# Performance work log

Hardware: AMD Instinct MI355X
Metric: run time of the kernel (lower is better)

## Reference

```python
import jax, jax.numpy as jnp
import numpy as np

B, D, T, R = 8, 128, 32768, 2
C = D // R  # reduced channel dim = 64


def conv1x1(x, w, b):
    # x: [B, Cin, T], w: [Cout, Cin], b: [Cout] -> [B, Cout, T]
    return jnp.einsum('oi,bit->bot', w, x) + b[None, :, None]


def setup_inputs() -> dict:
    key = jax.random.key(0)
    ks = jax.random.split(key, 16)
    inp = {
        'x1': jax.random.normal(ks[0], (B, D, T), dtype=jnp.float32),
        'x2': jnp.zeros((B, D, T), dtype=jnp.float32),  # unused in encoder stage
        'mask': jnp.ones((B, 1, T), dtype=jnp.float32),
        # 1x1 conv projections (weights squeezed to [out, in])
        'wq': jax.random.normal(ks[1], (C, D), dtype=jnp.float32) * 0.05,
        'bq': jnp.zeros((C,), dtype=jnp.float32),
        'wk': jax.random.normal(ks[2], (C, D), dtype=jnp.float32) * 0.05,
        'bk': jnp.zeros((C,), dtype=jnp.float32),
        'wv': jax.random.normal(ks[3], (C, D), dtype=jnp.float32) * 0.05,
        'bv': jnp.zeros((C,), dtype=jnp.float32),
        # E, F: Linear(C -> C) with bias
        'we': jax.random.normal(ks[4], (C, C), dtype=jnp.float32) * 0.1,
        'be': jnp.zeros((C,), dtype=jnp.float32),
        'wf': jax.random.normal(ks[5], (C, C), dtype=jnp.float32) * 0.1,
        'bf': jnp.zeros((C,), dtype=jnp.float32),
        # output 1x1 conv: C -> D
        'wo': jax.random.normal(ks[6], (D, C), dtype=jnp.float32) * 0.05,
        'bo': jnp.zeros((D,), dtype=jnp.float32),
    }
    return inp


def reference(x1, x2, mask, wq, bq, wk, bk, wv, bv, we, be, wf, bf, wo, bo):
    # Q/K/V projections (encoder stage: value from x1; x2 unused)
    Q = conv1x1(x1, wq, bq)              # [B, C, T]
    K = conv1x1(x1, wk, bk)              # [B, C, T]
    V = conv1x1(x1, wv, bv)              # [B, C, T]
    # K = E(K^T): [B, T, C] @ we^T + be
    Kp = jnp.einsum('bct,oc->bto', K, we) + be  # [B, T, C]
    # S = Q @ Kp -> [B, C, C], scaled by sqrt(last dim)
    S = jnp.einsum('bct,btk->bck', Q, Kp)
    P = jax.nn.softmax(S / jnp.sqrt(jnp.asarray(S.shape[-1], S.dtype)), axis=-1)
    # dropout is identity in eval mode
    # V = (F(V^T))^T: [B, C, T]
    Vp = jnp.einsum('bct,oc->bot', V, wf) + bf[None, :, None]  # [B, C, T]
    out = jnp.einsum('bck,bkt->bct', P, Vp)  # [B, C, T]
    out = conv1x1(jax.nn.relu(out), wo, bo)  # [B, D, T]
    return out * mask[:, 0:1, :]
```

## Files before the change

kernel.cpp:

```cpp
#include <hip/hip_runtime.h>
#include <stdint.h>
#include <stddef.h>

#define B_ 8
#define D_ 128
#define T_ 32768
#define C_ 64
#define NCH_ 128

typedef __bf16 bf16;
typedef __bf16 bf16x4 __attribute__((ext_vector_type(4)));
typedef __bf16 bf16x8 __attribute__((ext_vector_type(8)));
typedef float f32x2 __attribute__((ext_vector_type(2)));
typedef float f32x4 __attribute__((ext_vector_type(4)));
typedef float f32x16 __attribute__((ext_vector_type(16)));

__device__ __forceinline__ f32x16 zero16() {
  f32x16 z;
#pragma unroll
  for (int i = 0; i < 16; ++i) z[i] = 0.f;
  return z;
}

__global__ __launch_bounds__(256) void k0_zero(float* __restrict__ p, int n)
{
  int i = blockIdx.x * 256 + threadIdx.x;
  if (i < n) p[i] = 0.f;
}

__global__ __launch_bounds__(256, 2) void k1_gram(
    const float* __restrict__ x1,
    const float* __restrict__ we, const float* __restrict__ wk,
    const float* __restrict__ bk, const float* __restrict__ be,
    const float* __restrict__ wf, const float* __restrict__ wv,
    const float* __restrict__ bv, const float* __restrict__ bfv,
    const float* __restrict__ wo,
    float* __restrict__ G, float* __restrict__ r,
    float* __restrict__ wkp, float* __restrict__ wvp,
    float* __restrict__ bkp, float* __restrict__ bvp,
    bf16* __restrict__ wobf,
    float* __restrict__ gpart)
{
  const int blk = blockIdx.x;
  const int tid = threadIdx.x;
  const int ngram = B_ * NCH_;

  if (blk >= ngram) {
    const int wb = blk - ngram;
    if (wb < 64) {
      const float* wa  = (wb < 32) ? we : wf;
      const float* wb2 = (wb < 32) ? wk : wv;
      float* outw      = (wb < 32) ? wkp : wvp;
      const int idx = (wb & 31) * 256 + tid;
      const int o = idx >> 7, d = idx & 127;
      float s = 0.f;
      for (int c = 0; c < 64; ++c) s += wa[o * 64 + c] * wb2[c * 128 + d];
      outw[idx] = s;
      if (tid < 64) {
        if (wb == 0) {
          float t = 0.f;
          for (int c = 0; c < 64; ++c) t += we[tid * 64 + c] * bk[c];
          bkp[tid] = t + be[tid];
        } else if (wb == 32) {
          float t = 0.f;
          for (int c = 0; c < 64; ++c) t += wf[tid * 64 + c] * bv[c];
          bvp[tid] = t + bfv[tid];
        }
      }
    } else {
      const int idx = (wb - 64) * 256 + tid;
      wobf[idx] = (bf16)wo[idx];
    }
    return;
  }

  __shared__ bf16 x_s[128 * 264];

  const int b  = blk >> 7;
  const int ch = blk & (NCH_ - 1);
  const int t0 = ch * (T_ / NCH_);
  const int wave = tid >> 6, lane = tid & 63;
  const int lrow = lane & 31, lk = lane >> 5;
  const int qa = wave >> 1, qb = wave & 1;

  const float* xb = x1 + (size_t)b * D_ * T_ + t0;

#pragma unroll
  for (int g = 0; g < 4; ++g) {
    f32x4 pre[8];
#pragma unroll
    for (int i = 0; i < 8; ++i) {
      const int row = 32 * wave + 8 * g + i;
      pre[i] = *(const f32x4*)(xb + (size_t)row * T_ + 4 * lane);
    }
#pragma unroll
    for (int i = 0; i < 8; ++i) {
      const int row = 32 * wave + 8 * g + i;
      bf16x4 h;
#pragma unroll
      for (int j = 0; j < 4; ++j) h[j] = (bf16)pre[i][j];
      *(bf16x4*)&x_s[row * 264 + 4 * lane] = h;
    }
  }
  __syncthreads();

  f32x16 acc00 = zero16(), acc01 = zero16(), acc10 = zero16(), acc11 = zero16();
  float rsum = 0.f;

  const bf16* A0  = &x_s[(64 * qa + lrow) * 264 + 8 * lk];
  const bf16* A1  = A0 + 32 * 264;
  const bf16* Bb0 = &x_s[(64 * qb + lrow) * 264 + 8 * lk];
  const bf16* Bb1 = Bb0 + 32 * 264;

#pragma unroll
  for (int k = 0; k < 16; ++k) {
    bf16x8 fa0 = *(const bf16x8*)(A0 + 16 * k);
    bf16x8 fa1 = *(const bf16x8*)(A1 + 16 * k);
    bf16x8 fb0 = *(const bf16x8*)(Bb0 + 16 * k);
    bf16x8 fb1 = *(const bf16x8*)(Bb1 + 16 * k);
    bf16x8 own = qb ? fa1 : fa0;
#pragma unroll
    for (int j = 0; j < 8; ++j) rsum += (float)own[j];
    acc00 = __builtin_amdgcn_mfma_f32_32x32x16_bf16(fa0, fb0, acc00, 0, 0, 0);
    acc01 = __builtin_amdgcn_mfma_f32_32x32x16_bf16(fa0, fb1, acc01, 0, 0, 0);
    acc10 = __builtin_amdgcn_mfma_f32_32x32x16_bf16(fa1, fb0, acc10, 0, 0, 0);
    acc11 = __builtin_amdgcn_mfma_f32_32x32x16_bf16(fa1, fb1, acc11, 0, 0, 0);
  }

  if (gpart) {
    float* gp = gpart + (size_t)blk * 16384 + wave * 4096;
#pragma unroll
    for (int rr = 0; rr < 16; ++rr) {
      f32x4 v;
      v[0] = acc00[rr]; v[1] = acc01[rr]; v[2] = acc10[rr]; v[3] = acc11[rr];
      *(f32x4*)(gp + rr * 256 + lane * 4) = v;
    }
  } else {
    float* gb = G + (size_t)b * 16384;
#pragma unroll
    for (int rr = 0; rr < 16; ++rr) {
      const int rloc = (rr & 3) + 8 * (rr >> 2) + 4 * lk;
      const int r0 = 64 * qa + rloc, r1 = 64 * qa + 32 + rloc;
      const int c0 = 64 * qb + lrow, c1 = 64 * qb + 32 + lrow;
      atomicAdd(&gb[r0 * 128 + c0], acc00[rr]);
      atomicAdd(&gb[r0 * 128 + c1], acc01[rr]);
      atomicAdd(&gb[r1 * 128 + c0], acc10[rr]);
      atomicAdd(&gb[r1 * 128 + c1], acc11[rr]);
    }
  }
  float rtot = rsum + __shfl_xor(rsum, 32, 64);
  if (lk == 0) atomicAdd(&r[b * 128 + 32 * wave + lrow], rtot);
}

__global__ __launch_bounds__(256) void k2_reduce(
    const float* __restrict__ gpart, float* __restrict__ G)
{
  const int g4 = blockIdx.x * 256 + threadIdx.x;
  const int b = g4 >> 12;
  const int e4 = g4 & 4095;
  const f32x4* p = (const f32x4*)(gpart + ((size_t)b * NCH_) * 16384) + e4;
  f32x4 s = {0.f, 0.f, 0.f, 0.f};
#pragma unroll 8
  for (int ch = 0; ch < NCH_; ++ch) s += p[(size_t)ch * 4096];

  const int w = e4 >> 10, rr = (e4 >> 6) & 15, lane = e4 & 63;
  const int lk = lane >> 5, lrow = lane & 31;
  const int qa = w >> 1, qb = w & 1;
  const int rloc = (rr & 3) + 8 * (rr >> 2) + 4 * lk;
  const int r0 = 64 * qa + rloc, c0 = 64 * qb + lrow;
  float* Gb = G + (size_t)b * 16384;
  Gb[r0 * 128 + c0]               = s[0];
  Gb[r0 * 128 + c0 + 32]          = s[1];
  Gb[(r0 + 32) * 128 + c0]        = s[2];
  Gb[(r0 + 32) * 128 + c0 + 32]   = s[3];
}

__global__ __launch_bounds__(128) void k3_softmax(
    const float* __restrict__ wq, const float* __restrict__ bq,
    const float* __restrict__ G, const float* __restrict__ r,
    const float* __restrict__ wkp, const float* __restrict__ wvp,
    const float* __restrict__ bkp, const float* __restrict__ bvp,
    bf16* __restrict__ attw, float* __restrict__ attb)
{
  const int b = blockIdx.x >> 6, c = blockIdx.x & 63;
  const int tid = threadIdx.x;
  __shared__ float sM[128], sR[128], sQ[128], sP[64];
  __shared__ float sRed;

  const float* Gb = G + (size_t)b * 16384;
  const float* wqc = wq + c * 128;

  const float rv = r[b * 128 + tid];
  sR[tid] = rv;
  float m = 0.f;
  for (int j = 0; j < 128; ++j) m += wqc[j] * Gb[j * 128 + tid];
  sM[tid] = m;
  sQ[tid] = wqc[tid] * rv;
  __syncthreads();

  if (tid < 64) {
    float q2 = sQ[tid] + sQ[tid + 64];
#pragma unroll
    for (int off = 32; off; off >>= 1) q2 += __shfl_xor(q2, off, 64);
    if (tid == 0) sRed = q2;
  }
  __syncthreads();
  const float qr = sRed;
  const float bqc = bq[c];

  if (tid < 64) {
    const int k = tid;
    float s = 0.f, wkr = 0.f;
    for (int i = 0; i < 128; ++i) {
      const float w = wkp[k * 128 + i];
      s += sM[i] * w;
      wkr += sR[i] * w;
    }
    const float bk2 = bkp[k];
    float logit = (s + bqc * wkr + bk2 * qr + (float)T_ * bqc * bk2) * 0.125f;
    float mx = logit;
#pragma unroll
    for (int off = 32; off; off >>= 1) mx = fmaxf(mx, __shfl_xor(mx, off, 64));
    const float e = __expf(logit - mx);
    float sum = e;
#pragma unroll
    for (int off = 32; off; off >>= 1) sum += __shfl_xor(sum, off, 64);
    sP[k] = e / sum;
  }
  __syncthreads();

  {
    float aw = 0.f;
    for (int k = 0; k < 64; ++k) aw += sP[k] * wvp[k * 128 + tid];
    attw[((size_t)b * 64 + c) * 128 + tid] = (bf16)aw;
  }
  if (tid < 64) {
    float pb = sP[tid] * bvp[tid];
#pragma unroll
    for (int off = 32; off; off >>= 1) pb += __shfl_xor(pb, off, 64);
    if (tid == 0) attb[b * 64 + c] = pb;
  }
}

__global__ __launch_bounds__(256, 2) void k4_out(
    const float* __restrict__ x1, const float* __restrict__ mask,
    const bf16* __restrict__ wobf, const float* __restrict__ bo,
    const bf16* __restrict__ attw, const float* __restrict__ attb,
    float* __restrict__ out)
{
  __shared__ __attribute__((aligned(16))) char buf[128 * 136 * 2];
  bf16*  x_st = (bf16*)buf;
  float* o_s  = (float*)buf;
  __shared__ bf16 m1t[128 * 72];
  __shared__ float bo_s[128];
  __shared__ float ab_s[64];

  const int b = blockIdx.x >> 8;
  const int t0 = (blockIdx.x & 255) << 7;
  const int tid = threadIdx.x;
  const int wave = tid >> 6, lane = tid & 63;
  const int lrow = lane & 31, lk = lane >> 5;

  if (tid < 128) bo_s[tid] = bo[tid];
  if (tid < 64) ab_s[tid] = attb[b * 64 + tid];

  const float* xb = x1 + (size_t)b * D_ * T_ + t0;
#pragma unroll
  for (int g = 0; g < 4; ++g) {
    f32x2 pr[8];
#pragma unroll
    for (int i = 0; i < 8; ++i) {
      const int d = 32 * wave + 8 * g + i;
      pr[i] = *(const f32x2*)(xb + (size_t)d * T_ + 2 * lane);
    }
#pragma unroll
    for (int i = 0; i < 8; ++i) {
      const int d = 32 * wave + 8 * g + i;
      x_st[(2 * lane) * 136 + d]     = (bf16)pr[i][0];
      x_st[(2 * lane + 1) * 136 + d] = (bf16)pr[i][1];
    }
  }
  __syncthreads();

  const bf16* awb = attw + (size_t)b * 8192;
  f32x16 m0 = zero16(), m1a = zero16();
  const bf16* ax = &x_st[(32 * wave + lrow) * 136 + 8 * lk];
#pragma unroll
  for (int ki = 0; ki < 8; ++ki) {
    bf16x8 af = *(const bf16x8*)(ax + 16 * ki);
    bf16x8 b0 = *(const bf16x8*)(awb + (size_t)lrow * 128 + 16 * ki + 8 * lk);
    bf16x8 b1 = *(const bf16x8*)(awb + (size_t)(32 + lrow) * 128 + 16 * ki + 8 * lk);
    m0  = __builtin_amdgcn_mfma_f32_32x32x16_bf16(af, b0, m0, 0, 0, 0);
    m1a = __builtin_amdgcn_mfma_f32_32x32x16_bf16(af, b1, m1a, 0, 0, 0);
  }
#pragma unroll
  for (int rr = 0; rr < 16; ++rr) {
    const int tl = 32 * wave + (rr & 3) + 8 * (rr >> 2) + 4 * lk;
    m1t[tl * 72 + lrow]      = (bf16)fmaxf(m0[rr]  + ab_s[lrow], 0.f);
    m1t[tl * 72 + 32 + lrow] = (bf16)fmaxf(m1a[rr] + ab_s[32 + lrow], 0.f);
  }
  __syncthreads();

  f32x16 q0 = zero16(), q1 = zero16(), q2 = zero16(), q3 = zero16();
  const bf16* mrow = &m1t[(32 * wave + lrow) * 72];
#pragma unroll
  for (int k0 = 0; k0 < 4; ++k0) {
    bf16x8 bm = *(const bf16x8*)(mrow + 16 * k0 + 8 * lk);
    bf16x8 w0 = *(const bf16x8*)(wobf + (size_t)(lrow) * 64 + 16 * k0 + 8 * lk);
    bf16x8 w1 = *(const bf16x8*)(wobf + (size_t)(32 + lrow) * 64 + 16 * k0 + 8 * lk);
    bf16x8 w2 = *(const bf16x8*)(wobf + (size_t)(64 + lrow) * 64 + 16 * k0 + 8 * lk);
    bf16x8 w3 = *(const bf16x8*)(wobf + (size_t)(96 + lrow) * 64 + 16 * k0 + 8 * lk);
    q0 = __builtin_amdgcn_mfma_f32_32x32x16_bf16(w0, bm, q0, 0, 0, 0);
    q1 = __builtin_amdgcn_mfma_f32_32x32x16_bf16(w1, bm, q1, 0, 0, 0);
    q2 = __builtin_amdgcn_mfma_f32_32x32x16_bf16(w2, bm, q2, 0, 0, 0);
    q3 = __builtin_amdgcn_mfma_f32_32x32x16_bf16(w3, bm, q3, 0, 0, 0);
  }

  const int tl = 32 * wave + lrow;
  const float mv = mask[(size_t)b * T_ + t0 + tl];
  float* ob = out + (size_t)b * D_ * T_ + t0;

#pragma unroll
  for (int rr = 0; rr < 16; ++rr) {
    const int rloc = (rr & 3) + 8 * (rr >> 2) + 4 * lk;
    o_s[rloc * 132 + tl]        = (q0[rr] + bo_s[rloc]) * mv;
    o_s[(32 + rloc) * 132 + tl] = (q1[rr] + bo_s[32 + rloc]) * mv;
  }
  __syncthreads();
#pragma unroll
  for (int i = 0; i < 16; ++i) {
    const int dl = 16 * wave + i;
    f32x2 v = *(const f32x2*)(o_s + dl * 132 + 2 * lane);
    *(f32x2*)(ob + (size_t)dl * T_ + 2 * lane) = v;
  }
  __syncthreads();

#pragma unroll
  for (int rr = 0; rr < 16; ++rr) {
    const int rloc = (rr & 3) + 8 * (rr >> 2) + 4 * lk;
    o_s[rloc * 132 + tl]        = (q2[rr] + bo_s[64 + rloc]) * mv;
    o_s[(32 + rloc) * 132 + tl] = (q3[rr] + bo_s[96 + rloc]) * mv;
  }
  __syncthreads();
#pragma unroll
  for (int i = 0; i < 16; ++i) {
    const int dl = 16 * wave + i;
    f32x2 v = *(const f32x2*)(o_s + dl * 132 + 2 * lane);
    *(f32x2*)(ob + (size_t)(64 + dl) * T_ + 2 * lane) = v;
  }
}

extern "C" void kernel_launch(void* const* d_in, const int* in_sizes, int n_in,
                              void* d_out, int out_size, void* d_ws, size_t ws_size,
                              hipStream_t stream)
{
  const float* x1   = (const float*)d_in[0];
  const float* mask = (const float*)d_in[2];
  const float* wq   = (const float*)d_in[3];
  const float* bq   = (const float*)d_in[4];
  const float* wk   = (const float*)d_in[5];
  const float* bk   = (const float*)d_in[6];
  const float* wv   = (const float*)d_in[7];
  const float* bv   = (const float*)d_in[8];
  const float* we   = (const float*)d_in[9];
  const float* be   = (const float*)d_in[10];
  const float* wf   = (const float*)d_in[11];
  const float* bfv  = (const float*)d_in[12];
  const float* wo   = (const float*)d_in[13];
  const float* bo   = (const float*)d_in[14];
  float* out = (float*)d_out;

  char* base = (char*)d_ws;
  size_t off = 0;
  float* G    = (float*)(base + off); off += (size_t)B_ * 16384 * 4;
  float* r    = (float*)(base + off); off += (size_t)B_ * 128 * 4;
  float* wkp  = (float*)(base + off); off += 8192 * 4;
  float* wvp  = (float*)(base + off); off += 8192 * 4;
  float* bkp  = (float*)(base + off); off += 64 * 4;
  float* bvp  = (float*)(base + off); off += 64 * 4;
  float* attb = (float*)(base + off); off += (size_t)B_ * 64 * 4;
  bf16* attw  = (bf16*)(base + off);  off += (size_t)B_ * 64 * 128 * 2;
  bf16* wobf  = (bf16*)(base + off);  off += 8192 * 2;
  off = (off + 15) & ~(size_t)15;
  float* gpart = (float*)(base + off);
  const size_t need = off + (size_t)B_ * NCH_ * 16384 * 4;
  const bool use_part = (ws_size >= need);
  if (!use_part) gpart = nullptr;

  if (use_part) {
    k0_zero<<<(B_ * 128 + 255) / 256, 256, 0, stream>>>(r, B_ * 128);
  } else {
    const int nzero = B_ * 16384 + B_ * 128;
    k0_zero<<<(nzero + 255) / 256, 256, 0, stream>>>(G, nzero);
  }
  k1_gram<<<B_ * NCH_ + 96, 256, 0, stream>>>(
      x1, we, wk, bk, be, wf, wv, bv, bfv, wo,
      G, r, wkp, wvp, bkp, bvp, wobf, gpart);
  if (use_part)
    k2_reduce<<<(B_ * 16384) / (256 * 4), 256, 0, stream>>>(gpart, G);
  k3_softmax<<<B_ * 64, 128, 0, stream>>>(wq, bq, G, r, wkp, wvp, bkp, bvp, attw, attb);
  k4_out<<<B_ * (T_ / 128), 256, 0, stream>>>(x1, mask, wobf, bo, attw, attb, out);
}
```

Baseline: 394.9 us.

## Halve Gram chunk count and feed x directly into output-stage MFMA

The Gram kernel now uses half as many time chunks. Each block loops over two 256-wide sub-tiles staged through the same LDS buffer, which halves the number of partial Gram tiles or atomics to reduce. The output kernel drops the LDS transpose of x: each lane gathers its bf16 MFMA operand straight from global memory with strided scalar loads. Intermediate and output staging now share one smaller LDS buffer, and launch bounds rise to 4 blocks per CU. The trade-off is fewer, longer Gram blocks with an extra barrier, and many scalar global loads in place of vectorized ones.

```diff
diff --git a/kernel.cpp b/kernel.cpp
--- a/kernel.cpp
+++ b/kernel.cpp
@@ -6,7 +6,7 @@
 #define D_ 128
 #define T_ 32768
 #define C_ 64
-#define NCH_ 128
+#define NCH_ 64
 
 typedef __bf16 bf16;
 typedef __bf16 bf16x4 __attribute__((ext_vector_type(4)));
@@ -76,7 +76,7 @@
 
   __shared__ bf16 x_s[128 * 264];
 
-  const int b  = blk >> 7;
+  const int b  = blk / NCH_;
   const int ch = blk & (NCH_ - 1);
   const int t0 = ch * (T_ / NCH_);
   const int wave = tid >> 6, lane = tid & 63;
@@ -85,25 +85,6 @@
 
   const float* xb = x1 + (size_t)b * D_ * T_ + t0;
 
-#pragma unroll
-  for (int g = 0; g < 4; ++g) {
-    f32x4 pre[8];
-#pragma unroll
-    for (int i = 0; i < 8; ++i) {
-      const int row = 32 * wave + 8 * g + i;
-      pre[i] = *(const f32x4*)(xb + (size_t)row * T_ + 4 * lane);
-    }
-#pragma unroll
-    for (int i = 0; i < 8; ++i) {
-      const int row = 32 * wave + 8 * g + i;
-      bf16x4 h;
-#pragma unroll
-      for (int j = 0; j < 4; ++j) h[j] = (bf16)pre[i][j];
-      *(bf16x4*)&x_s[row * 264 + 4 * lane] = h;
-    }
-  }
-  __syncthreads();
-
   f32x16 acc00 = zero16(), acc01 = zero16(), acc10 = zero16(), acc11 = zero16();
   float rsum = 0.f;
 
@@ -112,19 +93,41 @@
   const bf16* Bb0 = &x_s[(64 * qb + lrow) * 264 + 8 * lk];
   const bf16* Bb1 = Bb0 + 32 * 264;
 
-#pragma unroll
-  for (int k = 0; k < 16; ++k) {
-    bf16x8 fa0 = *(const bf16x8*)(A0 + 16 * k);
-    bf16x8 fa1 = *(const bf16x8*)(A1 + 16 * k);
-    bf16x8 fb0 = *(const bf16x8*)(Bb0 + 16 * k);
-    bf16x8 fb1 = *(const bf16x8*)(Bb1 + 16 * k);
-    bf16x8 own = qb ? fa1 : fa0;
-#pragma unroll
-    for (int j = 0; j < 8; ++j) rsum += (float)own[j];
-    acc00 = __builtin_amdgcn_mfma_f32_32x32x16_bf16(fa0, fb0, acc00, 0, 0, 0);
-    acc01 = __builtin_amdgcn_mfma_f32_32x32x16_bf16(fa0, fb1, acc01, 0, 0, 0);
-    acc10 = __builtin_amdgcn_mfma_f32_32x32x16_bf16(fa1, fb0, acc10, 0, 0, 0);
-    acc11 = __builtin_amdgcn_mfma_f32_32x32x16_bf16(fa1, fb1, acc11, 0, 0, 0);
+  for (int s = 0; s < 2; ++s) {
+    const float* xs = xb + s * 256;
+    if (s) __syncthreads();
+#pragma unroll
+    for (int g = 0; g < 4; ++g) {
+      f32x4 pre[8];
+#pragma unroll
+      for (int i = 0; i < 8; ++i) {
+        const int row = 32 * wave + 8 * g + i;
+        pre[i] = *(const f32x4*)(xs + (size_t)row * T_ + 4 * lane);
+      }
+#pragma unroll
+      for (int i = 0; i < 8; ++i) {
+        const int row = 32 * wave + 8 * g + i;
+        bf16x4 h;
+#pragma unroll
+        for (int j = 0; j < 4; ++j) h[j] = (bf16)pre[i][j];
+        *(bf16x4*)&x_s[row * 264 + 4 * lane] = h;
+      }
+    }
+    __syncthreads();
+#pragma unroll
+    for (int k = 0; k < 16; ++k) {
+      bf16x8 fa0 = *(const bf16x8*)(A0 + 16 * k);
+      bf16x8 fa1 = *(const bf16x8*)(A1 + 16 * k);
+      bf16x8 fb0 = *(const bf16x8*)(Bb0 + 16 * k);
+      bf16x8 fb1 = *(const bf16x8*)(Bb1 + 16 * k);
+      bf16x8 own = qb ? fa1 : fa0;
+#pragma unroll
+      for (int j = 0; j < 8; ++j) rsum += (float)own[j];
+      acc00 = __builtin_amdgcn_mfma_f32_32x32x16_bf16(fa0, fb0, acc00, 0, 0, 0);
+      acc01 = __builtin_amdgcn_mfma_f32_32x32x16_bf16(fa0, fb1, acc01, 0, 0, 0);
+      acc10 = __builtin_amdgcn_mfma_f32_32x32x16_bf16(fa1, fb0, acc10, 0, 0, 0);
+      acc11 = __builtin_amdgcn_mfma_f32_32x32x16_bf16(fa1, fb1, acc11, 0, 0, 0);
+    }
   }
 
   if (gpart) {
@@ -242,16 +245,15 @@
   }
 }
 
-__global__ __launch_bounds__(256, 2) void k4_out(
+__global__ __launch_bounds__(256, 4) void k4_out(
     const float* __restrict__ x1, const float* __restrict__ mask,
     const bf16* __restrict__ wobf, const float* __restrict__ bo,
     const bf16* __restrict__ attw, const float* __restrict__ attb,
     float* __restrict__ out)
 {
-  __shared__ __attribute__((aligned(16))) char buf[128 * 136 * 2];
-  bf16*  x_st = (bf16*)buf;
-  float* o_s  = (float*)buf;
-  __shared__ bf16 m1t[128 * 72];
+  __shared__ __attribute__((aligned(16))) char ubuf[64 * 132 * 4];
+  bf16*  m1  = (bf16*)ubuf;
+  float* o_s = (float*)ubuf;
   __shared__ float bo_s[128];
   __shared__ float ab_s[64];
 
@@ -260,49 +262,36 @@
   const int tid = threadIdx.x;
   const int wave = tid >> 6, lane = tid & 63;
   const int lrow = lane & 31, lk = lane >> 5;
+  const int tcol = 32 * wave + lrow;
 
   if (tid < 128) bo_s[tid] = bo[tid];
   if (tid < 64) ab_s[tid] = attb[b * 64 + tid];
-
-  const float* xb = x1 + (size_t)b * D_ * T_ + t0;
-#pragma unroll
-  for (int g = 0; g < 4; ++g) {
-    f32x2 pr[8];
-#pragma unroll
-    for (int i = 0; i < 8; ++i) {
-      const int d = 32 * wave + 8 * g + i;
-      pr[i] = *(const f32x2*)(xb + (size_t)d * T_ + 2 * lane);
-    }
-#pragma unroll
-    for (int i = 0; i < 8; ++i) {
-      const int d = 32 * wave + 8 * g + i;
-      x_st[(2 * lane) * 136 + d]     = (bf16)pr[i][0];
-      x_st[(2 * lane + 1) * 136 + d] = (bf16)pr[i][1];
-    }
-  }
-  __syncthreads();
-
+  __syncthreads();
+
+  const float* xc = x1 + (size_t)b * D_ * T_ + t0 + tcol;
   const bf16* awb = attw + (size_t)b * 8192;
-  f32x16 m0 = zero16(), m1a = zero16();
-  const bf16* ax = &x_st[(32 * wave + lrow) * 136 + 8 * lk];
-#pragma unroll
-  for (int ki = 0; ki < 8; ++ki) {
-    bf16x8 af = *(const bf16x8*)(ax + 16 * ki);
-    bf16x8 b0 = *(const bf16x8*)(awb + (size_t)lrow * 128 + 16 * ki + 8 * lk);
-    bf16x8 b1 = *(const bf16x8*)(awb + (size_t)(32 + lrow) * 128 + 16 * ki + 8 * lk);
-    m0  = __builtin_amdgcn_mfma_f32_32x32x16_bf16(af, b0, m0, 0, 0, 0);
-    m1a = __builtin_amdgcn_mfma_f32_32x32x16_bf16(af, b1, m1a, 0, 0, 0);
-  }
+
+  f32x16 p0 = zero16(), p1 = zero16();
+#pragma unroll
+  for (int k0 = 0; k0 < 8; ++k0) {
+    bf16x8 a0 = *(const bf16x8*)(awb + (size_t)lrow * 128 + 16 * k0 + 8 * lk);
+    bf16x8 a1 = *(const bf16x8*)(awb + (size_t)(32 + lrow) * 128 + 16 * k0 + 8 * lk);
+    bf16x8 bx;
+#pragma unroll
+    for (int j = 0; j < 8; ++j)
+      bx[j] = (bf16)xc[(size_t)(16 * k0 + 8 * lk + j) * T_];
+    p0 = __builtin_amdgcn_mfma_f32_32x32x16_bf16(a0, bx, p0, 0, 0, 0);
+    p1 = __builtin_amdgcn_mfma_f32_32x32x16_bf16(a1, bx, p1, 0, 0, 0);
+  }
+  bf16* mrow = &m1[tcol * 72];
 #pragma unroll
   for (int rr = 0; rr < 16; ++rr) {
-    const int tl = 32 * wave + (rr & 3) + 8 * (rr >> 2) + 4 * lk;
-    m1t[tl * 72 + lrow]      = (bf16)fmaxf(m0[rr]  + ab_s[lrow], 0.f);
-    m1t[tl * 72 + 32 + lrow] = (bf16)fmaxf(m1a[rr] + ab_s[32 + lrow], 0.f);
-  }
-  __syncthreads();
+    const int row = (rr & 3) + 8 * (rr >> 2) + 4 * lk;
+    mrow[row]      = (bf16)fmaxf(p0[rr] + ab_s[row], 0.f);
+    mrow[32 + row] = (bf16)fmaxf(p1[rr] + ab_s[32 + row], 0.f);
+  }
 
   f32x16 q0 = zero16(), q1 = zero16(), q2 = zero16(), q3 = zero16();
-  const bf16* mrow = &m1t[(32 * wave + lrow) * 72];
 #pragma unroll
   for (int k0 = 0; k0 < 4; ++k0) {
     bf16x8 bm = *(const bf16x8*)(mrow + 16 * k0 + 8 * lk);
@@ -316,15 +305,15 @@
     q3 = __builtin_amdgcn_mfma_f32_32x32x16_bf16(w3, bm, q3, 0, 0, 0);
   }
 
-  const int tl = 32 * wave + lrow;
-  const float mv = mask[(size_t)b * T_ + t0 + tl];
+  const float mv = mask[(size_t)b * T_ + t0 + tcol];
   float* ob = out + (size_t)b * D_ * T_ + t0;
 
+  __syncthreads();
 #pragma unroll
   for (int rr = 0; rr < 16; ++rr) {
     const int rloc = (rr & 3) + 8 * (rr >> 2) + 4 * lk;
-    o_s[rloc * 132 + tl]        = (q0[rr] + bo_s[rloc]) * mv;
-    o_s[(32 + rloc) * 132 + tl] = (q1[rr] + bo_s[32 + rloc]) * mv;
+    o_s[rloc * 132 + tcol]        = (q0[rr] + bo_s[rloc]) * mv;
+    o_s[(32 + rloc) * 132 + tcol] = (q1[rr] + bo_s[32 + rloc]) * mv;
   }
   __syncthreads();
 #pragma unroll
@@ -334,12 +323,11 @@
     *(f32x2*)(ob + (size_t)dl * T_ + 2 * lane) = v;
   }
   __syncthreads();
-
 #pragma unroll
   for (int rr = 0; rr < 16; ++rr) {
     const int rloc = (rr & 3) + 8 * (rr >> 2) + 4 * lk;
-    o_s[rloc * 132 + tl]        = (q2[rr] + bo_s[64 + rloc]) * mv;
-    o_s[(32 + rloc) * 132 + tl] = (q3[rr] + bo_s[96 + rloc]) * mv;
+    o_s[rloc * 132 + tcol]        = (q2[rr] + bo_s[64 + rloc]) * mv;
+    o_s[(32 + rloc) * 132 + tcol] = (q3[rr] + bo_s[96 + rloc]) * mv;
   }
   __syncthreads();
 #pragma unroll
```

After: 375.7 us. 1.05x faster.
